# Kernel optimization log

Measured on AMD Instinct MI355X. Metric: run time of the kernel, lower is better.

## Reference

```python
import jax, jax.numpy as jnp
import numpy as np

FEATURE_HEIGHT = 50
FEATURE_WIDTH = 50


def setup_inputs() -> dict:
    key = jax.random.key(0)
    k1, k2, k3 = jax.random.split(key, 3)
    bs, K, H, D = 16, FEATURE_HEIGHT * FEATURE_WIDTH, 8, 32
    Q, L, P = 2000, 1, 4
    value = jax.random.normal(k1, (bs, K, H, D), dtype=jnp.float32)
    value_spatial_shapes = jnp.array([[FEATURE_HEIGHT, FEATURE_WIDTH]], dtype=jnp.int64)
    sampling_locations = jax.random.uniform(k2, (bs, Q, H, L, P, 2), dtype=jnp.float32)
    attention_weights = jax.random.uniform(k3, (bs, Q, H, L, P), dtype=jnp.float32)
    return {
        "value": value,
        "value_spatial_shapes": value_spatial_shapes,
        "sampling_locations": sampling_locations,
        "attention_weights": attention_weights,
    }


def _bilinear_sample(img, grid):
    """torch.F.grid_sample(mode='bilinear', padding_mode='zeros', align_corners=False).

    img:  (N, D, h, w)
    grid: (N, Q, P, 2), last dim (x, y) in [-1, 1]
    returns (N, D, Q, P)
    """
    N, D, h, w = img.shape
    # unnormalize (align_corners=False)
    x = (grid[..., 0] + 1.0) * (w * 0.5) - 0.5  # (N, Q, P)
    y = (grid[..., 1] + 1.0) * (h * 0.5) - 0.5
    x0 = jnp.floor(x)
    y0 = jnp.floor(y)
    x1 = x0 + 1.0
    y1 = y0 + 1.0
    wx1 = x - x0
    wx0 = 1.0 - wx1
    wy1 = y - y0
    wy0 = 1.0 - wy1

    img_flat = img.reshape(N, D, h * w)

    def corner(ix, iy, wgt):
        valid = ((ix >= 0) & (ix < w) & (iy >= 0) & (iy < h)).astype(img.dtype)
        ixc = jnp.clip(ix, 0, w - 1).astype(jnp.int32)
        iyc = jnp.clip(iy, 0, h - 1).astype(jnp.int32)
        idx = (iyc * w + ixc).reshape(N, -1)  # (N, Q*P)
        vals = jnp.take_along_axis(img_flat, idx[:, None, :], axis=2)  # (N, D, Q*P)
        vals = vals.reshape(N, D, *ix.shape[1:])  # (N, D, Q, P)
        return vals * (wgt * valid)[:, None]

    out = corner(x0, y0, wx0 * wy0)
    out = out + corner(x1, y0, wx1 * wy0)
    out = out + corner(x0, y1, wx0 * wy1)
    out = out + corner(x1, y1, wx1 * wy1)
    return out


def reference(value, value_spatial_shapes, sampling_locations, attention_weights):
    bs, K, H, D = value.shape
    _, Q, _, L, P, _ = sampling_locations.shape
    h, w = FEATURE_HEIGHT, FEATURE_WIDTH

    sampling_grids = 2.0 * sampling_locations - 1.0  # (bs, Q, H, L, P, 2)
    # value -> (bs*H, D, h, w)
    v = value.reshape(bs, K, H * D).transpose(0, 2, 1).reshape(bs * H, D, h, w)
    # level 0 grid -> (bs*H, Q, P, 2)
    g = jnp.transpose(sampling_grids[:, :, :, 0], (0, 2, 1, 3, 4)).reshape(bs * H, Q, P, 2)
    sampled = _bilinear_sample(v, g)  # (bs*H, D, Q, P)
    # attention weights -> (bs*H, 1, Q, L*P)
    aw = jnp.transpose(attention_weights, (0, 2, 1, 3, 4)).reshape(bs * H, 1, Q, L * P)
    out = (sampled * aw).sum(-1)  # (bs*H, D, Q)
    out = out.reshape(bs, H * D, Q).transpose(0, 2, 1)  # (bs, Q, H*D)
    return out
```

## Files before the change

kernel.cpp:

```cpp
#include <hip/hip_runtime.h>
#include <hip/hip_fp16.h>


#define FH 50
#define FW 50
#define KK (FH * FW)
#define NH 8
#define ND 32
#define NQ 2000
#define NP 4
#define QHALF 1000

__global__ __launch_bounds__(256, 4) void deform_attn_kernel(
    const float* __restrict__ value,
    const float* __restrict__ loc,
    const float* __restrict__ attw,
    float* __restrict__ out)
{
    const int blk = blockIdx.x;
    const int xcd = blk & 7;
    const int s = blk >> 3;
    const int cg = s >> 5;
    const int t5 = s & 31;
    const int bph = t5 >> 4;
    const int h = (t5 >> 1) & 7;
    const int qh = t5 & 1;
    const int b = xcd + (bph << 3);

    __shared__ ushort sv[KK * 8];
    {
        const float4* __restrict__ vsrc = (const float4*)value;
        const size_t vbase = (size_t)b * KK * 64 + h * 8 + cg * 2;
        for (int i = threadIdx.x; i < 2 * KK; i += 256) {
            const int k = i >> 1;
            const int halfsel = i & 1;
            const float4 f = vsrc[vbase + (size_t)k * 64 + halfsel];
            const __half2 p0 = __floats2half2_rn(f.x, f.y);
            const __half2 p1 = __floats2half2_rn(f.z, f.w);
            uint2 packed;
            packed.x = *(const unsigned int*)&p0;
            packed.y = *(const unsigned int*)&p1;
            *((uint2*)&sv[k * 8 + halfsel * 4]) = packed;
        }
    }
    __syncthreads();

    const float4* __restrict__ loc4 = (const float4*)loc;
    const float4* __restrict__ attw4 = (const float4*)attw;
    float4* __restrict__ out4 = (float4*)out;

    for (int r = 0; r < 4; ++r) {
        const int ql = r * 256 + threadIdx.x;
        if (ql >= QHALF) break;
        const int q = qh * QHALF + ql;
        const int gid = (b * NQ + q) * NH + h;

        const float4 l0 = loc4[(size_t)gid * 2];
        const float4 l1 = loc4[(size_t)gid * 2 + 1];
        const float4 a4 = attw4[gid];

        const float pxx[NP] = {l0.x, l0.z, l1.x, l1.z};
        const float pyy[NP] = {l0.y, l0.w, l1.y, l1.w};
        const float awp[NP] = {a4.x, a4.y, a4.z, a4.w};

        int offs[16];
        float wts[16];
#pragma unroll
        for (int p = 0; p < NP; ++p) {
            const float fx = pxx[p] * (float)FW - 0.5f;
            const float fy = pyy[p] * (float)FH - 0.5f;
            const float x0f = floorf(fx);
            const float y0f = floorf(fy);
            const int x0 = (int)x0f, y0 = (int)y0f;
            const int x1 = x0 + 1, y1 = y0 + 1;
            const float wx1 = fx - x0f, wx0 = 1.f - wx1;
            const float wy1 = fy - y0f, wy0 = 1.f - wy1;

            const bool vx0 = (x0 >= 0) & (x0 < FW);
            const bool vx1 = (x1 >= 0) & (x1 < FW);
            const bool vy0 = (y0 >= 0) & (y0 < FH);
            const bool vy1 = (y1 >= 0) & (y1 < FH);

            const int cx0 = min(max(x0, 0), FW - 1);
            const int cx1 = min(max(x1, 0), FW - 1);
            const int cy0 = min(max(y0, 0), FH - 1);
            const int cy1 = min(max(y1, 0), FH - 1);

            offs[p * 4 + 0] = (cy0 * FW + cx0) * 8;
            offs[p * 4 + 1] = (cy0 * FW + cx1) * 8;
            offs[p * 4 + 2] = (cy1 * FW + cx0) * 8;
            offs[p * 4 + 3] = (cy1 * FW + cx1) * 8;

            wts[p * 4 + 0] = ((vx0 & vy0) ? (wx0 * wy0) : 0.f) * awp[p];
            wts[p * 4 + 1] = ((vx1 & vy0) ? (wx1 * wy0) : 0.f) * awp[p];
            wts[p * 4 + 2] = ((vx0 & vy1) ? (wx0 * wy1) : 0.f) * awp[p];
            wts[p * 4 + 3] = ((vx1 & vy1) ? (wx1 * wy1) : 0.f) * awp[p];
        }

        float a0 = 0.f, a1 = 0.f, a2 = 0.f, a3 = 0.f;
        float a4_ = 0.f, a5 = 0.f, a6 = 0.f, a7 = 0.f;
#pragma unroll
        for (int i = 0; i < 16; ++i) {
            const uint4 rv = *((const uint4*)&sv[offs[i]]);
            const float w = wts[i];
            const float2 f0 = __half22float2(*(const __half2*)&rv.x);
            const float2 f1 = __half22float2(*(const __half2*)&rv.y);
            const float2 f2 = __half22float2(*(const __half2*)&rv.z);
            const float2 f3 = __half22float2(*(const __half2*)&rv.w);
            a0 += w * f0.x; a1 += w * f0.y;
            a2 += w * f1.x; a3 += w * f1.y;
            a4_ += w * f2.x; a5 += w * f2.y;
            a6 += w * f3.x; a7 += w * f3.y;
        }

        const size_t o = (size_t)(b * NQ + q) * 64 + h * 8 + cg * 2;
        out4[o] = make_float4(a0, a1, a2, a3);
        out4[o + 1] = make_float4(a4_, a5, a6, a7);
    }
}

extern "C" void kernel_launch(void* const* d_in, const int* in_sizes, int n_in,
                              void* d_out, int out_size, void* d_ws, size_t ws_size,
                              hipStream_t stream) {
    const float* value = (const float*)d_in[0];
    const float* loc  = (const float*)d_in[2];
    const float* attw = (const float*)d_in[3];
    float* out = (float*)d_out;

    deform_attn_kernel<<<1024, 256, 0, stream>>>(value, loc, attw, out);
}
```

Baseline: 129.3 us.

## Stage all channels per head in LDS and split channels across threads

Each block now loads the full 32-channel fp16 value map for one batch/head into 160 KB of dynamic shared memory and uses 1024 threads, with 8 threads per query each producing 4 channels. This removes the fourfold recomputation of sampling offsets, bilinear weights and location/attention loads that came from splitting channels across separate blocks. In exchange the grid shrinks to one large block per CU, so staging cannot overlap with compute from other blocks and occupancy depends on a single block.

```diff
diff --git a/kernel.cpp b/kernel.cpp
--- a/kernel.cpp
+++ b/kernel.cpp
@@ -11,46 +11,48 @@
 #define NP 4
 #define QHALF 1000
 
-__global__ __launch_bounds__(256, 4) void deform_attn_kernel(
+__global__ __launch_bounds__(1024, 4) void deform_attn_kernel(
     const float* __restrict__ value,
     const float* __restrict__ loc,
     const float* __restrict__ attw,
     float* __restrict__ out)
 {
+    extern __shared__ ushort sv[];
+
     const int blk = blockIdx.x;
     const int xcd = blk & 7;
     const int s = blk >> 3;
-    const int cg = s >> 5;
-    const int t5 = s & 31;
-    const int bph = t5 >> 4;
-    const int h = (t5 >> 1) & 7;
-    const int qh = t5 & 1;
+    const int bph = s >> 4;
+    const int h = (s >> 1) & 7;
+    const int qh = s & 1;
     const int b = xcd + (bph << 3);
 
-    __shared__ ushort sv[KK * 8];
     {
         const float4* __restrict__ vsrc = (const float4*)value;
-        const size_t vbase = (size_t)b * KK * 64 + h * 8 + cg * 2;
-        for (int i = threadIdx.x; i < 2 * KK; i += 256) {
-            const int k = i >> 1;
-            const int halfsel = i & 1;
-            const float4 f = vsrc[vbase + (size_t)k * 64 + halfsel];
+        const size_t vbase = (size_t)b * KK * 64 + h * 8;
+        for (int i = threadIdx.x; i < KK * 8; i += 1024) {
+            const int k = i >> 3;
+            const int c = i & 7;
+            const float4 f = vsrc[vbase + (size_t)k * 64 + c];
             const __half2 p0 = __floats2half2_rn(f.x, f.y);
             const __half2 p1 = __floats2half2_rn(f.z, f.w);
             uint2 packed;
             packed.x = *(const unsigned int*)&p0;
             packed.y = *(const unsigned int*)&p1;
-            *((uint2*)&sv[k * 8 + halfsel * 4]) = packed;
+            *((uint2*)&sv[(size_t)i * 4]) = packed;
         }
     }
     __syncthreads();
+
+    const int c = threadIdx.x & 7;
+    const int grp = threadIdx.x >> 3;
 
     const float4* __restrict__ loc4 = (const float4*)loc;
     const float4* __restrict__ attw4 = (const float4*)attw;
     float4* __restrict__ out4 = (float4*)out;
 
-    for (int r = 0; r < 4; ++r) {
-        const int ql = r * 256 + threadIdx.x;
+    for (int j = 0; j < 8; ++j) {
+        const int ql = j * 128 + grp;
         if (ql >= QHALF) break;
         const int q = qh * QHALF + ql;
         const int gid = (b * NQ + q) * NH + h;
@@ -86,10 +88,10 @@
             const int cy0 = min(max(y0, 0), FH - 1);
             const int cy1 = min(max(y1, 0), FH - 1);
 
-            offs[p * 4 + 0] = (cy0 * FW + cx0) * 8;
-            offs[p * 4 + 1] = (cy0 * FW + cx1) * 8;
-            offs[p * 4 + 2] = (cy1 * FW + cx0) * 8;
-            offs[p * 4 + 3] = (cy1 * FW + cx1) * 8;
+            offs[p * 4 + 0] = (cy0 * FW + cx0) * 32 + c * 4;
+            offs[p * 4 + 1] = (cy0 * FW + cx1) * 32 + c * 4;
+            offs[p * 4 + 2] = (cy1 * FW + cx0) * 32 + c * 4;
+            offs[p * 4 + 3] = (cy1 * FW + cx1) * 32 + c * 4;
 
             wts[p * 4 + 0] = ((vx0 & vy0) ? (wx0 * wy0) : 0.f) * awp[p];
             wts[p * 4 + 1] = ((vx1 & vy0) ? (wx1 * wy0) : 0.f) * awp[p];
@@ -98,24 +100,18 @@
         }
 
         float a0 = 0.f, a1 = 0.f, a2 = 0.f, a3 = 0.f;
-        float a4_ = 0.f, a5 = 0.f, a6 = 0.f, a7 = 0.f;
 #pragma unroll
         for (int i = 0; i < 16; ++i) {
-            const uint4 rv = *((const uint4*)&sv[offs[i]]);
+            const uint2 rv = *((const uint2*)&sv[offs[i]]);
             const float w = wts[i];
             const float2 f0 = __half22float2(*(const __half2*)&rv.x);
             const float2 f1 = __half22float2(*(const __half2*)&rv.y);
-            const float2 f2 = __half22float2(*(const __half2*)&rv.z);
-            const float2 f3 = __half22float2(*(const __half2*)&rv.w);
             a0 += w * f0.x; a1 += w * f0.y;
             a2 += w * f1.x; a3 += w * f1.y;
-            a4_ += w * f2.x; a5 += w * f2.y;
-            a6 += w * f3.x; a7 += w * f3.y;
         }
 
-        const size_t o = (size_t)(b * NQ + q) * 64 + h * 8 + cg * 2;
-        out4[o] = make_float4(a0, a1, a2, a3);
-        out4[o + 1] = make_float4(a4_, a5, a6, a7);
+        out4[(size_t)(b * NQ + q) * 64 + h * 8 + c] =
+            make_float4(a0, a1, a2, a3);
     }
 }
 
@@ -127,5 +123,9 @@
     const float* attw = (const float*)d_in[3];
     float* out = (float*)d_out;
 
-    deform_attn_kernel<<<1024, 256, 0, stream>>>(value, loc, attw, out);
+    static_assert(KK * 32 * sizeof(ushort) == 160000, "LDS size");
+    hipFuncSetAttribute((const void*)deform_attn_kernel,
+                        hipFuncAttributeMaxDynamicSharedMemorySize, 160000);
+
+    deform_attn_kernel<<<256, 1024, 160000, stream>>>(value, loc, attw, out);
 }
```

New measurement: 120.6 us. -6.7%, faster.
